# Kernel tuning notes

Hardware: AMD Instinct MI355X
Metric: run time of the kernel (lower is better)

## Reference

```python
import jax, jax.numpy as jnp
import numpy as np

N, E = 50000, 640000          # nodes, edges
F_IN, HID, CLS = 128, 128, 64  # feature dims


def setup_inputs() -> dict:
    key = jax.random.key(0)
    ks = jax.random.split(key, 12)
    x = jax.random.normal(ks[0], (N, F_IN), dtype=jnp.float32)
    edge_index = jax.random.randint(ks[1], (2, E), 0, N, dtype=jnp.int32)
    s_in = 1.0 / np.sqrt(F_IN)
    s_h = 1.0 / np.sqrt(HID)
    return {
        "x": x,
        "edge_index": edge_index,
        "W0": jax.random.normal(ks[2], (F_IN, HID), jnp.float32) * s_in,
        "b0": jnp.zeros((HID,), jnp.float32),
        "W1": jax.random.normal(ks[3], (HID, HID), jnp.float32) * s_h,
        "b1": jnp.zeros((HID,), jnp.float32),
        "W2": jax.random.normal(ks[4], (HID, HID), jnp.float32) * s_h,
        "b2": jnp.zeros((HID,), jnp.float32),
        "W_lin": jax.random.normal(ks[5], (HID, CLS), jnp.float32) * s_h,
        "b_lin": jnp.zeros((CLS,), jnp.float32),
    }


def reference(x, edge_index, W0, b0, W1, b1, W2, b2, W_lin, b_lin):
    # GCNConv (PyG defaults): out = D^-1/2 (A + I) D^-1/2 (x @ W) + b
    row, col = edge_index[0], edge_index[1]  # source -> target
    # degree with self-loop (graph is fixed across layers, compute norms once)
    deg = jnp.zeros((N,), x.dtype).at[col].add(1.0) + 1.0
    dinv = jax.lax.rsqrt(deg)                 # deg >= 1, safe
    enorm = (dinv[row] * dinv[col])[:, None]  # [E,1] edge norm
    snorm = (dinv * dinv)[:, None]            # [N,1] self-loop norm

    def conv(h, W, b):
        h = h @ W                                             # [N,HID]
        agg = jnp.zeros_like(h).at[col].add(h[row] * enorm)   # neighbor agg
        return agg + h * snorm + b                            # + self loop + bias

    h = jax.nn.relu(conv(x, W0, b0))
    h = jax.nn.relu(conv(h, W1, b1))
    h = jax.nn.relu(conv(h, W2, b2))
    return h @ W_lin + b_lin
```

## Files before the change

kernel.cpp:

```cpp
#include <hip/hip_runtime.h>
#include <hip/hip_fp16.h>

#define N_NODES 50000
#define HID 128
#define CLS 64

#define NBINS 196
#define NBLK 256
#define LBUF_CAP 4096
#define WTOT 57344
#define GEMM0_BLOCKS 782
#define AROW 136

typedef __attribute__((ext_vector_type(8))) _Float16 f16x8;
typedef __attribute__((ext_vector_type(4))) float f32x4;

__global__ __launch_bounds__(256) void hist_wsplit_kernel(
    const int* __restrict__ col, int* __restrict__ hist,
    const float* __restrict__ W0, const float* __restrict__ W1,
    const float* __restrict__ W2, const float* __restrict__ Wl,
    __half* __restrict__ o0h, __half* __restrict__ o0l,
    __half* __restrict__ o1h, __half* __restrict__ o1l,
    __half* __restrict__ o2h, __half* __restrict__ o2l,
    __half* __restrict__ o3h, __half* __restrict__ o3l,
    int E, int chunk) {
    int widx = blockIdx.x * 256 + threadIdx.x;
    if (widx < WTOT) {
        const float* W;
        __half *oh, *ol;
        int NCdim, local;
        if (widx < 16384)      { W = W0; oh = o0h; ol = o0l; NCdim = 128; local = widx; }
        else if (widx < 32768) { W = W1; oh = o1h; ol = o1l; NCdim = 128; local = widx - 16384; }
        else if (widx < 49152) { W = W2; oh = o2h; ol = o2l; NCdim = 128; local = widx - 32768; }
        else                   { W = Wl; oh = o3h; ol = o3l; NCdim = 64;  local = widx - 49152; }
        int nn = local >> 7;
        int k = local & 127;
        float v = W[(size_t)k * NCdim + nn];
        __half h = __float2half_rn(v);
        oh[local] = h;
        ol[local] = __float2half_rn(v - __half2float(h));
    }
    __shared__ int h[NBINS];
    for (int i = threadIdx.x; i < NBINS; i += 256) h[i] = 0;
    __syncthreads();
    int b = blockIdx.x;
    int beg = b * chunk;
    int end = min(E, beg + chunk);
    if (beg < end) {
        int vend = beg + ((end - beg) & ~3);
        for (int i = beg + threadIdx.x * 4; i < vend; i += 1024) {
            int4 c4 = *(const int4*)(col + i);
            atomicAdd(&h[c4.x >> 8], 1);
            atomicAdd(&h[c4.y >> 8], 1);
            atomicAdd(&h[c4.z >> 8], 1);
            atomicAdd(&h[c4.w >> 8], 1);
        }
        int i = vend + threadIdx.x;
        if (i < end) atomicAdd(&h[col[i] >> 8], 1);
    }
    __syncthreads();
    for (int i = threadIdx.x; i < NBINS; i += 256)
        hist[i * NBLK + b] = h[i];
}

__global__ __launch_bounds__(256) void binscan_kernel(
    const int* __restrict__ hist, int* __restrict__ cursorBase,
    int* __restrict__ binTotal) {
    __shared__ int ss[256];
    int bin = blockIdx.x, t = threadIdx.x;
    int v = hist[bin * NBLK + t];
    ss[t] = v;
    __syncthreads();
#pragma unroll
    for (int off = 1; off < 256; off <<= 1) {
        int u = (t >= off) ? ss[t - off] : 0;
        __syncthreads();
        ss[t] += u;
        __syncthreads();
    }
    cursorBase[bin * NBLK + t] = ss[t] - v;
    if (t == 255) binTotal[bin] = ss[255];
}

__global__ __launch_bounds__(256) void scatter_kernel(
    const int* __restrict__ row, const int* __restrict__ col,
    const int* __restrict__ binTotal, const int* __restrict__ cursorBase,
    int* __restrict__ binBase_g,
    unsigned short* __restrict__ sbuf_src, unsigned char* __restrict__ sbuf_c,
    int E, int chunk) {
    __shared__ int ss[256];
    __shared__ int cur[NBINS];
    int b = blockIdx.x, t = threadIdx.x;
    int v = (t < NBINS) ? binTotal[t] : 0;
    ss[t] = v;
    __syncthreads();
#pragma unroll
    for (int off = 1; off < 256; off <<= 1) {
        int u = (t >= off) ? ss[t - off] : 0;
        __syncthreads();
        ss[t] += u;
        __syncthreads();
    }
    int myBase = ss[t] - v;
    if (t < NBINS) cur[t] = myBase + cursorBase[t * NBLK + b];
    if (b == 0) {
        if (t < NBINS) binBase_g[t] = myBase;
        if (t == 0) binBase_g[NBINS] = E;
    }
    __syncthreads();
    int beg = b * chunk;
    int end = min(E, beg + chunk);
    if (beg >= end) return;
    int vend = beg + ((end - beg) & ~3);
    for (int i = beg + t * 4; i < vend; i += 1024) {
        int4 c4 = *(const int4*)(col + i);
        int4 r4 = *(const int4*)(row + i);
        int p;
        p = atomicAdd(&cur[c4.x >> 8], 1); sbuf_src[p] = (unsigned short)r4.x; sbuf_c[p] = (unsigned char)(c4.x & 255);
        p = atomicAdd(&cur[c4.y >> 8], 1); sbuf_src[p] = (unsigned short)r4.y; sbuf_c[p] = (unsigned char)(c4.y & 255);
        p = atomicAdd(&cur[c4.z >> 8], 1); sbuf_src[p] = (unsigned short)r4.z; sbuf_c[p] = (unsigned char)(c4.z & 255);
        p = atomicAdd(&cur[c4.w >> 8], 1); sbuf_src[p] = (unsigned short)r4.w; sbuf_c[p] = (unsigned char)(c4.w & 255);
    }
    int i = vend + t;
    if (i < end) {
        int c = col[i];
        int p = atomicAdd(&cur[c >> 8], 1);
        sbuf_src[p] = (unsigned short)row[i];
        sbuf_c[p] = (unsigned char)(c & 255);
    }
}

__device__ __forceinline__ void gemm0_body(
    const float* __restrict__ x, const __half* __restrict__ Bh,
    const __half* __restrict__ Bl, __half* __restrict__ C, int M, int rowTile) {
    constexpr int NT = 8;
    int lane = threadIdx.x & 63;
    int m0 = rowTile << 4;
    if (m0 >= M) return;
    int mr = lane & 15;
    int kq = (lane >> 4) << 3;

    const float*  af = x + (size_t)(m0 + mr) * 128 + kq;
    const __half* bh = Bh + (size_t)mr * 128 + kq;
    const __half* bl = Bl + (size_t)mr * 128 + kq;

    f32x4 acc[NT];
#pragma unroll
    for (int t = 0; t < NT; ++t) acc[t] = (f32x4){0.f, 0.f, 0.f, 0.f};
#pragma unroll
    for (int kc = 0; kc < 128; kc += 32) {
        float4 lo = *(const float4*)(af + kc);
        float4 hi = *(const float4*)(af + kc + 4);
        f16x8 a;
        a[0] = (_Float16)lo.x; a[1] = (_Float16)lo.y;
        a[2] = (_Float16)lo.z; a[3] = (_Float16)lo.w;
        a[4] = (_Float16)hi.x; a[5] = (_Float16)hi.y;
        a[6] = (_Float16)hi.z; a[7] = (_Float16)hi.w;
#pragma unroll
        for (int t = 0; t < NT; ++t) {
            f16x8 wh = *(const f16x8*)(bh + (size_t)t * 16 * 128 + kc);
            f16x8 wl = *(const f16x8*)(bl + (size_t)t * 16 * 128 + kc);
            acc[t] = __builtin_amdgcn_mfma_f32_16x16x32_f16(a, wh, acc[t], 0, 0, 0);
            acc[t] = __builtin_amdgcn_mfma_f32_16x16x32_f16(a, wl, acc[t], 0, 0, 0);
        }
    }
    int r0 = m0 + ((lane >> 4) << 2);
    int cc = lane & 15;
#pragma unroll
    for (int t = 0; t < NT; ++t)
#pragma unroll
        for (int r = 0; r < 4; ++r)
            C[(size_t)(r0 + r) * 128 + t * 16 + cc] =
                __float2half_rn(acc[t][r]);
}

__global__ __launch_bounds__(256) void csrplace_gemm0_kernel(
    const int* __restrict__ binBase,
    const unsigned short* __restrict__ sbuf_src, const unsigned char* __restrict__ sbuf_c,
    float* __restrict__ dinv, int* __restrict__ row_ptr,
    unsigned short* __restrict__ csr_src,
    const float* __restrict__ x, const __half* __restrict__ W0h,
    const __half* __restrict__ W0l, __half* __restrict__ h2, int n, int E) {
    __shared__ int lcnt[256];
    __shared__ int lcur[256];
    __shared__ int ss[256];
    __shared__ int lbuf[LBUF_CAP];
    int b = blockIdx.x;
    if (b >= NBINS) {
        gemm0_body(x, W0h, W0l, h2, n, (b - NBINS) * 4 + (threadIdx.x >> 6));
        return;
    }
    int t = threadIdx.x;
    lcnt[t] = 0;
    __syncthreads();
    int beg = binBase[b], end = binBase[b + 1];
    for (int j = beg + t; j < end; j += 256)
        atomicAdd(&lcnt[sbuf_c[j]], 1);
    __syncthreads();
    int deg = lcnt[t];
    int node = b * 256 + t;
    if (node < n) dinv[node] = rsqrtf((float)deg + 1.0f);
    ss[t] = deg;
    __syncthreads();
#pragma unroll
    for (int off = 1; off < 256; off <<= 1) {
        int u = (t >= off) ? ss[t - off] : 0;
        __syncthreads();
        ss[t] += u;
        __syncthreads();
    }
    int excl = ss[t] - deg;
    lcur[t] = excl;
    int total = ss[255];
    if (node < n) row_ptr[node] = beg + excl;
    if (b == 0 && t == 0) row_ptr[n] = E;
    __syncthreads();
    for (int j = beg + t; j < end; j += 256) {
        int c = sbuf_c[j];
        int pos = atomicAdd(&lcur[c], 1);
        lbuf[pos] = sbuf_src[j];
    }
    __syncthreads();
    for (int j = t; j < total; j += 256)
        csr_src[beg + j] = (unsigned short)lbuf[j];
}

template<int NC, bool HEAD>
__global__ __launch_bounds__(256) void agg_gemm_kernel(
    const __half* __restrict__ h2, const int* __restrict__ row_ptr,
    const unsigned short* __restrict__ csr_src, const float* __restrict__ dinv,
    const float* __restrict__ bias,
    const __half* __restrict__ Bh, const __half* __restrict__ Bl,
    const float* __restrict__ gbias, void* __restrict__ Cv, int n) {
    __shared__ __half Als[16][AROW];
    int wave = threadIdx.x >> 6;
    int lane = threadIdx.x & 63;
    int m0 = blockIdx.x << 4;

    int g = lane >> 4;
    int l16 = lane & 15;
    int baseLane = lane & 48;
    int lr = (wave << 2) + g;
    int wid = m0 + lr;
    const __half* hrow = h2 + (l16 << 3);

    if (wid < n) {
        int beg = row_ptr[wid];
        int end = row_ptr[wid + 1];
        float dv = dinv[wid];
        float acc[8];
#pragma unroll
        for (int i = 0; i < 8; ++i) acc[i] = 0.f;

        for (int base = beg; base < end; base += 16) {
            int cnt = end - base;
            if (cnt > 16) cnt = 16;
            int msrc = 0;
            float mw = 0.f;
            if (l16 < cnt) {
                msrc = csr_src[base + l16];
                mw = dinv[msrc] * dv;
            }
            int j = 0;
            for (; j + 4 <= cnt; j += 4) {
                int s0 = __shfl(msrc, baseLane + j);
                int s1 = __shfl(msrc, baseLane + j + 1);
                int s2 = __shfl(msrc, baseLane + j + 2);
                int s3 = __shfl(msrc, baseLane + j + 3);
                float w0 = __shfl(mw, baseLane + j);
                float w1 = __shfl(mw, baseLane + j + 1);
                float w2 = __shfl(mw, baseLane + j + 2);
                float w3 = __shfl(mw, baseLane + j + 3);
                f16x8 v0 = *(const f16x8*)(hrow + ((size_t)s0 << 7));
                f16x8 v1 = *(const f16x8*)(hrow + ((size_t)s1 << 7));
                f16x8 v2 = *(const f16x8*)(hrow + ((size_t)s2 << 7));
                f16x8 v3 = *(const f16x8*)(hrow + ((size_t)s3 << 7));
#pragma unroll
                for (int i = 0; i < 8; ++i) {
                    acc[i] = fmaf((float)v0[i], w0, acc[i]);
                    acc[i] = fmaf((float)v1[i], w1, acc[i]);
                    acc[i] = fmaf((float)v2[i], w2, acc[i]);
                    acc[i] = fmaf((float)v3[i], w3, acc[i]);
                }
            }
            for (; j + 2 <= cnt; j += 2) {
                int s0 = __shfl(msrc, baseLane + j);
                int s1 = __shfl(msrc, baseLane + j + 1);
                float w0 = __shfl(mw, baseLane + j);
                float w1 = __shfl(mw, baseLane + j + 1);
                f16x8 v0 = *(const f16x8*)(hrow + ((size_t)s0 << 7));
                f16x8 v1 = *(const f16x8*)(hrow + ((size_t)s1 << 7));
#pragma unroll
                for (int i = 0; i < 8; ++i) {
                    acc[i] = fmaf((float)v0[i], w0, acc[i]);
                    acc[i] = fmaf((float)v1[i], w1, acc[i]);
                }
            }
            if (j < cnt) {
                int s0 = __shfl(msrc, baseLane + j);
                float w0 = __shfl(mw, baseLane + j);
                f16x8 v0 = *(const f16x8*)(hrow + ((size_t)s0 << 7));
#pragma unroll
                for (int i = 0; i < 8; ++i)
                    acc[i] = fmaf((float)v0[i], w0, acc[i]);
            }
        }
        float sn = dv * dv;
        f16x8 sv = *(const f16x8*)(hrow + ((size_t)wid << 7));
        float4 ba = *(const float4*)(bias + (l16 << 3));
        float4 bb = *(const float4*)(bias + (l16 << 3) + 4);
        float o[8];
#pragma unroll
        for (int i = 0; i < 8; ++i) o[i] = fmaf((float)sv[i], sn, acc[i]);
        o[0] += ba.x; o[1] += ba.y; o[2] += ba.z; o[3] += ba.w;
        o[4] += bb.x; o[5] += bb.y; o[6] += bb.z; o[7] += bb.w;
        f16x8 pk;
#pragma unroll
        for (int i = 0; i < 8; ++i) pk[i] = (_Float16)fmaxf(o[i], 0.f);
        *(f16x8*)&Als[lr][l16 << 3] = pk;
    }
    __syncthreads();

    constexpr int NT = NC / 16;
    constexpr int TPW = NT / 4;
    int mr = lane & 15;
    int kq = (lane >> 4) << 3;
    const __half* bh = Bh + (size_t)mr * 128 + kq;
    const __half* bl = Bl + (size_t)mr * 128 + kq;

    f32x4 acc[TPW];
#pragma unroll
    for (int t = 0; t < TPW; ++t) acc[t] = (f32x4){0.f, 0.f, 0.f, 0.f};
#pragma unroll
    for (int kc = 0; kc < 128; kc += 32) {
        f16x8 a = *(const f16x8*)&Als[mr][kq + kc];
#pragma unroll
        for (int t = 0; t < TPW; ++t) {
            int tile = wave * TPW + t;
            f16x8 wh = *(const f16x8*)(bh + (size_t)tile * 16 * 128 + kc);
            f16x8 wl = *(const f16x8*)(bl + (size_t)tile * 16 * 128 + kc);
            acc[t] = __builtin_amdgcn_mfma_f32_16x16x32_f16(a, wh, acc[t], 0, 0, 0);
            acc[t] = __builtin_amdgcn_mfma_f32_16x16x32_f16(a, wl, acc[t], 0, 0, 0);
        }
    }
    int r0 = m0 + ((lane >> 4) << 2);
    int cc = lane & 15;
#pragma unroll
    for (int t = 0; t < TPW; ++t) {
        int tile = wave * TPW + t;
        float bsv = HEAD ? gbias[tile * 16 + cc] : 0.f;
#pragma unroll
        for (int r = 0; r < 4; ++r) {
            if (r0 + r >= n) break;
            size_t idx = (size_t)(r0 + r) * NC + tile * 16 + cc;
            float val = acc[t][r] + bsv;
            if (HEAD)
                ((float*)Cv)[idx] = val;
            else
                ((__half*)Cv)[idx] = __float2half_rn(val);
        }
    }
}

extern "C" void kernel_launch(void* const* d_in, const int* in_sizes, int n_in,
                              void* d_out, int out_size, void* d_ws, size_t ws_size,
                              hipStream_t stream) {
    const float* x  = (const float*)d_in[0];
    const int* ei   = (const int*)d_in[1];
    const float* W0 = (const float*)d_in[2];
    const float* b0 = (const float*)d_in[3];
    const float* W1 = (const float*)d_in[4];
    const float* b1 = (const float*)d_in[5];
    const float* W2 = (const float*)d_in[6];
    const float* b2 = (const float*)d_in[7];
    const float* Wl = (const float*)d_in[8];
    const float* bl = (const float*)d_in[9];
    float* out = (float*)d_out;

    const int N = N_NODES;
    const int E = in_sizes[1] / 2;
    const int* row = ei;
    const int* col = ei + E;
    const int chunk = (((E + NBLK - 1) / NBLK) + 3) & ~3;

    char* ws = (char*)d_ws;
    auto alloc = [&](size_t bytes) {
        char* p = ws;
        ws += (bytes + 255) & ~(size_t)255;
        return p;
    };
    int*   hist      = (int*)alloc((size_t)NBINS * NBLK * 4);
    int*   cursorBase= (int*)alloc((size_t)NBINS * NBLK * 4);
    int*   binTotal  = (int*)alloc((size_t)NBINS * 4);
    int*   binBase   = (int*)alloc((size_t)(NBINS + 1) * 4);
    unsigned short* sbuf_src = (unsigned short*)alloc((size_t)E * 2);
    unsigned char*  sbuf_c   = (unsigned char*)alloc((size_t)E);
    int*   row_ptr = (int*)alloc((size_t)(N + 1) * 4);
    float* dinv    = (float*)alloc((size_t)N * 4);
    unsigned short* csr_src = (unsigned short*)alloc((size_t)E * 2);
    __half* h2a    = (__half*)alloc((size_t)N * HID * 2);
    __half* h2b    = (__half*)alloc((size_t)N * HID * 2);
    __half* Wt_h[4];
    __half* Wt_l[4];
    for (int i = 0; i < 3; ++i) {
        Wt_h[i] = (__half*)alloc((size_t)HID * HID * 2);
        Wt_l[i] = (__half*)alloc((size_t)HID * HID * 2);
    }
    Wt_h[3] = (__half*)alloc((size_t)CLS * HID * 2);
    Wt_l[3] = (__half*)alloc((size_t)CLS * HID * 2);

    hist_wsplit_kernel<<<NBLK, 256, 0, stream>>>(col, hist, W0, W1, W2, Wl,
        Wt_h[0], Wt_l[0], Wt_h[1], Wt_l[1], Wt_h[2], Wt_l[2], Wt_h[3], Wt_l[3], E, chunk);
    binscan_kernel<<<NBINS, 256, 0, stream>>>(hist, cursorBase, binTotal);
    scatter_kernel<<<NBLK, 256, 0, stream>>>(row, col, binTotal, cursorBase,
        binBase, sbuf_src, sbuf_c, E, chunk);
    csrplace_gemm0_kernel<<<NBINS + GEMM0_BLOCKS, 256, 0, stream>>>(
        binBase, sbuf_src, sbuf_c, dinv, row_ptr, csr_src,
        x, Wt_h[0], Wt_l[0], h2a, N, E);

    const int fusedBlocks = (N + 15) / 16;

    agg_gemm_kernel<128, false><<<fusedBlocks, 256, 0, stream>>>(
        h2a, row_ptr, csr_src, dinv, b0, Wt_h[1], Wt_l[1], nullptr, h2b, N);
    agg_gemm_kernel<128, false><<<fusedBlocks, 256, 0, stream>>>(
        h2b, row_ptr, csr_src, dinv, b1, Wt_h[2], Wt_l[2], nullptr, h2a, N);
    agg_gemm_kernel<64, true><<<fusedBlocks, 256, 0, stream>>>(
        h2a, row_ptr, csr_src, dinv, b2, Wt_h[3], Wt_l[3], bl, out, N);
}
```

Baseline: 265.5 us.

## Replace binned two-level CSR build with global-atomic degree count and direct scatter

```diff
diff --git a/kernel.cpp b/kernel.cpp
--- a/kernel.cpp
+++ b/kernel.cpp
@@ -5,25 +5,24 @@
 #define HID 128
 #define CLS 64
 
-#define NBINS 196
-#define NBLK 256
-#define LBUF_CAP 4096
+#define NSCAN 196
 #define WTOT 57344
+#define SCAT_BLOCKS 256
 #define GEMM0_BLOCKS 782
 #define AROW 136
 
 typedef __attribute__((ext_vector_type(8))) _Float16 f16x8;
 typedef __attribute__((ext_vector_type(4))) float f32x4;
 
-__global__ __launch_bounds__(256) void hist_wsplit_kernel(
-    const int* __restrict__ col, int* __restrict__ hist,
+__global__ __launch_bounds__(256) void degcount_wsplit_kernel(
+    const int* __restrict__ col, int* __restrict__ deg,
     const float* __restrict__ W0, const float* __restrict__ W1,
     const float* __restrict__ W2, const float* __restrict__ Wl,
     __half* __restrict__ o0h, __half* __restrict__ o0l,
     __half* __restrict__ o1h, __half* __restrict__ o1l,
     __half* __restrict__ o2h, __half* __restrict__ o2l,
     __half* __restrict__ o3h, __half* __restrict__ o3l,
-    int E, int chunk) {
+    int E) {
     int widx = blockIdx.x * 256 + threadIdx.x;
     if (widx < WTOT) {
         const float* W;
@@ -40,35 +39,29 @@
         oh[local] = h;
         ol[local] = __float2half_rn(v - __half2float(h));
     }
-    __shared__ int h[NBINS];
-    for (int i = threadIdx.x; i < NBINS; i += 256) h[i] = 0;
-    __syncthreads();
-    int b = blockIdx.x;
-    int beg = b * chunk;
-    int end = min(E, beg + chunk);
-    if (beg < end) {
-        int vend = beg + ((end - beg) & ~3);
-        for (int i = beg + threadIdx.x * 4; i < vend; i += 1024) {
-            int4 c4 = *(const int4*)(col + i);
-            atomicAdd(&h[c4.x >> 8], 1);
-            atomicAdd(&h[c4.y >> 8], 1);
-            atomicAdd(&h[c4.z >> 8], 1);
-            atomicAdd(&h[c4.w >> 8], 1);
-        }
-        int i = vend + threadIdx.x;
-        if (i < end) atomicAdd(&h[col[i] >> 8], 1);
-    }
-    __syncthreads();
-    for (int i = threadIdx.x; i < NBINS; i += 256)
-        hist[i * NBLK + b] = h[i];
-}
-
-__global__ __launch_bounds__(256) void binscan_kernel(
-    const int* __restrict__ hist, int* __restrict__ cursorBase,
-    int* __restrict__ binTotal) {
+    int E4 = E & ~3;
+    int stride = 256 * 256 * 4;
+    for (int i = (blockIdx.x * 256 + threadIdx.x) * 4; i < E4; i += stride) {
+        int4 c4 = *(const int4*)(col + i);
+        atomicAdd(&deg[c4.x], 1);
+        atomicAdd(&deg[c4.y], 1);
+        atomicAdd(&deg[c4.z], 1);
+        atomicAdd(&deg[c4.w], 1);
+    }
+    if (blockIdx.x == 0) {
+        int r = E - E4;
+        if (threadIdx.x < r) atomicAdd(&deg[col[E4 + threadIdx.x]], 1);
+    }
+}
+
+__global__ __launch_bounds__(256) void scan_local_kernel(
+    const int* __restrict__ deg, int* __restrict__ rpl,
+    int* __restrict__ blockSum, float* __restrict__ dinv, int n) {
     __shared__ int ss[256];
-    int bin = blockIdx.x, t = threadIdx.x;
-    int v = hist[bin * NBLK + t];
+    int b = blockIdx.x, t = threadIdx.x;
+    int node = b * 256 + t;
+    int v = (node < n) ? deg[node] : 0;
+    if (node < n) dinv[node] = rsqrtf((float)v + 1.0f);
     ss[t] = v;
     __syncthreads();
 #pragma unroll
@@ -78,21 +71,19 @@
         ss[t] += u;
         __syncthreads();
     }
-    cursorBase[bin * NBLK + t] = ss[t] - v;
-    if (t == 255) binTotal[bin] = ss[255];
-}
-
-__global__ __launch_bounds__(256) void scatter_kernel(
-    const int* __restrict__ row, const int* __restrict__ col,
-    const int* __restrict__ binTotal, const int* __restrict__ cursorBase,
-    int* __restrict__ binBase_g,
-    unsigned short* __restrict__ sbuf_src, unsigned char* __restrict__ sbuf_c,
-    int E, int chunk) {
+    if (node < n) rpl[node] = ss[t] - v;
+    if (t == 255) blockSum[b] = ss[255];
+}
+
+__global__ __launch_bounds__(256) void scan_final_kernel(
+    const int* __restrict__ rpl, const int* __restrict__ blockSum,
+    int* __restrict__ row_ptr, int* __restrict__ cur, int n, int E) {
     __shared__ int ss[256];
-    __shared__ int cur[NBINS];
+    __shared__ int orig[256];
     int b = blockIdx.x, t = threadIdx.x;
-    int v = (t < NBINS) ? binTotal[t] : 0;
+    int v = (t < NSCAN) ? blockSum[t] : 0;
     ss[t] = v;
+    orig[t] = v;
     __syncthreads();
 #pragma unroll
     for (int off = 1; off < 256; off <<= 1) {
@@ -101,33 +92,14 @@
         ss[t] += u;
         __syncthreads();
     }
-    int myBase = ss[t] - v;
-    if (t < NBINS) cur[t] = myBase + cursorBase[t * NBLK + b];
-    if (b == 0) {
-        if (t < NBINS) binBase_g[t] = myBase;
-        if (t == 0) binBase_g[NBINS] = E;
-    }
-    __syncthreads();
-    int beg = b * chunk;
-    int end = min(E, beg + chunk);
-    if (beg >= end) return;
-    int vend = beg + ((end - beg) & ~3);
-    for (int i = beg + t * 4; i < vend; i += 1024) {
-        int4 c4 = *(const int4*)(col + i);
-        int4 r4 = *(const int4*)(row + i);
-        int p;
-        p = atomicAdd(&cur[c4.x >> 8], 1); sbuf_src[p] = (unsigned short)r4.x; sbuf_c[p] = (unsigned char)(c4.x & 255);
-        p = atomicAdd(&cur[c4.y >> 8], 1); sbuf_src[p] = (unsigned short)r4.y; sbuf_c[p] = (unsigned char)(c4.y & 255);
-        p = atomicAdd(&cur[c4.z >> 8], 1); sbuf_src[p] = (unsigned short)r4.z; sbuf_c[p] = (unsigned char)(c4.z & 255);
-        p = atomicAdd(&cur[c4.w >> 8], 1); sbuf_src[p] = (unsigned short)r4.w; sbuf_c[p] = (unsigned char)(c4.w & 255);
-    }
-    int i = vend + t;
-    if (i < end) {
-        int c = col[i];
-        int p = atomicAdd(&cur[c >> 8], 1);
-        sbuf_src[p] = (unsigned short)row[i];
-        sbuf_c[p] = (unsigned char)(c & 255);
-    }
+    int base = ss[b] - orig[b];
+    int node = b * 256 + t;
+    if (node < n) {
+        int r = rpl[node] + base;
+        row_ptr[node] = r;
+        cur[node] = r;
+    }
+    if (b == 0 && t == 0) row_ptr[n] = E;
 }
 
 __device__ __forceinline__ void gemm0_body(
@@ -174,55 +146,38 @@
                 __float2half_rn(acc[t][r]);
 }
 
-__global__ __launch_bounds__(256) void csrplace_gemm0_kernel(
-    const int* __restrict__ binBase,
-    const unsigned short* __restrict__ sbuf_src, const unsigned char* __restrict__ sbuf_c,
-    float* __restrict__ dinv, int* __restrict__ row_ptr,
-    unsigned short* __restrict__ csr_src,
+__global__ __launch_bounds__(256) void scatter_gemm0_kernel(
+    const int* __restrict__ row, const int* __restrict__ col,
+    int* __restrict__ cur, unsigned short* __restrict__ csr_src,
     const float* __restrict__ x, const __half* __restrict__ W0h,
     const __half* __restrict__ W0l, __half* __restrict__ h2, int n, int E) {
-    __shared__ int lcnt[256];
-    __shared__ int lcur[256];
-    __shared__ int ss[256];
-    __shared__ int lbuf[LBUF_CAP];
     int b = blockIdx.x;
-    if (b >= NBINS) {
-        gemm0_body(x, W0h, W0l, h2, n, (b - NBINS) * 4 + (threadIdx.x >> 6));
+    if (b >= SCAT_BLOCKS) {
+        gemm0_body(x, W0h, W0l, h2, n, (b - SCAT_BLOCKS) * 4 + (threadIdx.x >> 6));
         return;
     }
     int t = threadIdx.x;
-    lcnt[t] = 0;
-    __syncthreads();
-    int beg = binBase[b], end = binBase[b + 1];
-    for (int j = beg + t; j < end; j += 256)
-        atomicAdd(&lcnt[sbuf_c[j]], 1);
-    __syncthreads();
-    int deg = lcnt[t];
-    int node = b * 256 + t;
-    if (node < n) dinv[node] = rsqrtf((float)deg + 1.0f);
-    ss[t] = deg;
-    __syncthreads();
-#pragma unroll
-    for (int off = 1; off < 256; off <<= 1) {
-        int u = (t >= off) ? ss[t - off] : 0;
-        __syncthreads();
-        ss[t] += u;
-        __syncthreads();
-    }
-    int excl = ss[t] - deg;
-    lcur[t] = excl;
-    int total = ss[255];
-    if (node < n) row_ptr[node] = beg + excl;
-    if (b == 0 && t == 0) row_ptr[n] = E;
-    __syncthreads();
-    for (int j = beg + t; j < end; j += 256) {
-        int c = sbuf_c[j];
-        int pos = atomicAdd(&lcur[c], 1);
-        lbuf[pos] = sbuf_src[j];
-    }
-    __syncthreads();
-    for (int j = t; j < total; j += 256)
-        csr_src[beg + j] = (unsigned short)lbuf[j];
+    int E4 = E & ~3;
+    int stride = SCAT_BLOCKS * 256 * 4;
+    for (int i = (b * 256 + t) * 4; i < E4; i += stride) {
+        int4 c4 = *(const int4*)(col + i);
+        int4 r4 = *(const int4*)(row + i);
+        int p0 = atomicAdd(&cur[c4.x], 1);
+        int p1 = atomicAdd(&cur[c4.y], 1);
+        int p2 = atomicAdd(&cur[c4.z], 1);
+        int p3 = atomicAdd(&cur[c4.w], 1);
+        csr_src[p0] = (unsigned short)r4.x;
+        csr_src[p1] = (unsigned short)r4.y;
+        csr_src[p2] = (unsigned short)r4.z;
+        csr_src[p3] = (unsigned short)r4.w;
+    }
+    if (b == 0) {
+        int r = E - E4;
+        if (t < r) {
+            int p = atomicAdd(&cur[col[E4 + t]], 1);
+            csr_src[p] = (unsigned short)row[E4 + t];
+        }
+    }
 }
 
 template<int NC, bool HEAD>
@@ -381,7 +336,6 @@
     const int E = in_sizes[1] / 2;
     const int* row = ei;
     const int* col = ei + E;
-    const int chunk = (((E + NBLK - 1) / NBLK) + 3) & ~3;
 
     char* ws = (char*)d_ws;
     auto alloc = [&](size_t bytes) {
@@ -389,14 +343,12 @@
         ws += (bytes + 255) & ~(size_t)255;
         return p;
     };
-    int*   hist      = (int*)alloc((size_t)NBINS * NBLK * 4);
-    int*   cursorBase= (int*)alloc((size_t)NBINS * NBLK * 4);
-    int*   binTotal  = (int*)alloc((size_t)NBINS * 4);
-    int*   binBase   = (int*)alloc((size_t)(NBINS + 1) * 4);
-    unsigned short* sbuf_src = (unsigned short*)alloc((size_t)E * 2);
-    unsigned char*  sbuf_c   = (unsigned char*)alloc((size_t)E);
-    int*   row_ptr = (int*)alloc((size_t)(N + 1) * 4);
-    float* dinv    = (float*)alloc((size_t)N * 4);
+    int*   deg      = (int*)alloc((size_t)N * 4);
+    int*   rpl      = (int*)alloc((size_t)N * 4);
+    int*   blockSum = (int*)alloc((size_t)NSCAN * 4);
+    int*   row_ptr  = (int*)alloc((size_t)(N + 1) * 4);
+    int*   cur      = (int*)alloc((size_t)N * 4);
+    float* dinv     = (float*)alloc((size_t)N * 4);
     unsigned short* csr_src = (unsigned short*)alloc((size_t)E * 2);
     __half* h2a    = (__half*)alloc((size_t)N * HID * 2);
     __half* h2b    = (__half*)alloc((size_t)N * HID * 2);
@@ -409,14 +361,14 @@
     Wt_h[3] = (__half*)alloc((size_t)CLS * HID * 2);
     Wt_l[3] = (__half*)alloc((size_t)CLS * HID * 2);
 
-    hist_wsplit_kernel<<<NBLK, 256, 0, stream>>>(col, hist, W0, W1, W2, Wl,
-        Wt_h[0], Wt_l[0], Wt_h[1], Wt_l[1], Wt_h[2], Wt_l[2], Wt_h[3], Wt_l[3], E, chunk);
-    binscan_kernel<<<NBINS, 256, 0, stream>>>(hist, cursorBase, binTotal);
-    scatter_kernel<<<NBLK, 256, 0, stream>>>(row, col, binTotal, cursorBase,
-        binBase, sbuf_src, sbuf_c, E, chunk);
-    csrplace_gemm0_kernel<<<NBINS + GEMM0_BLOCKS, 256, 0, stream>>>(
-        binBase, sbuf_src, sbuf_c, dinv, row_ptr, csr_src,
-        x, Wt_h[0], Wt_l[0], h2a, N, E);
+    hipMemsetAsync(deg, 0, (size_t)N * 4, stream);
+
+    degcount_wsplit_kernel<<<256, 256, 0, stream>>>(col, deg, W0, W1, W2, Wl,
+        Wt_h[0], Wt_l[0], Wt_h[1], Wt_l[1], Wt_h[2], Wt_l[2], Wt_h[3], Wt_l[3], E);
+    scan_local_kernel<<<NSCAN, 256, 0, stream>>>(deg, rpl, blockSum, dinv, N);
+    scan_final_kernel<<<NSCAN, 256, 0, stream>>>(rpl, blockSum, row_ptr, cur, N, E);
+    scatter_gemm0_kernel<<<SCAT_BLOCKS + GEMM0_BLOCKS, 256, 0, stream>>>(
+        row, col, cur, csr_src, x, Wt_h[0], Wt_l[0], h2a, N, E);
 
     const int fusedBlocks = (N + 15) / 16;
 
```

Result: slower. 308.5 us (+16.2%).

## Move gemm0 blocks into histogram kernel and split weight conversion into own launch

Applied to the files above, without the earlier changes.

```diff
diff --git a/kernel.cpp b/kernel.cpp
--- a/kernel.cpp
+++ b/kernel.cpp
@@ -9,41 +9,93 @@
 #define NBLK 256
 #define LBUF_CAP 4096
 #define WTOT 57344
+#define WSPLIT_BLOCKS 224
 #define GEMM0_BLOCKS 782
 #define AROW 136
 
 typedef __attribute__((ext_vector_type(8))) _Float16 f16x8;
 typedef __attribute__((ext_vector_type(4))) float f32x4;
 
-__global__ __launch_bounds__(256) void hist_wsplit_kernel(
-    const int* __restrict__ col, int* __restrict__ hist,
+__global__ __launch_bounds__(256) void wsplit_kernel(
     const float* __restrict__ W0, const float* __restrict__ W1,
     const float* __restrict__ W2, const float* __restrict__ Wl,
     __half* __restrict__ o0h, __half* __restrict__ o0l,
     __half* __restrict__ o1h, __half* __restrict__ o1l,
     __half* __restrict__ o2h, __half* __restrict__ o2l,
-    __half* __restrict__ o3h, __half* __restrict__ o3l,
-    int E, int chunk) {
+    __half* __restrict__ o3h, __half* __restrict__ o3l) {
     int widx = blockIdx.x * 256 + threadIdx.x;
-    if (widx < WTOT) {
-        const float* W;
-        __half *oh, *ol;
-        int NCdim, local;
-        if (widx < 16384)      { W = W0; oh = o0h; ol = o0l; NCdim = 128; local = widx; }
-        else if (widx < 32768) { W = W1; oh = o1h; ol = o1l; NCdim = 128; local = widx - 16384; }
-        else if (widx < 49152) { W = W2; oh = o2h; ol = o2l; NCdim = 128; local = widx - 32768; }
-        else                   { W = Wl; oh = o3h; ol = o3l; NCdim = 64;  local = widx - 49152; }
-        int nn = local >> 7;
-        int k = local & 127;
-        float v = W[(size_t)k * NCdim + nn];
-        __half h = __float2half_rn(v);
-        oh[local] = h;
-        ol[local] = __float2half_rn(v - __half2float(h));
+    const float* W;
+    __half *oh, *ol;
+    int NCdim, local;
+    if (widx < 16384)      { W = W0; oh = o0h; ol = o0l; NCdim = 128; local = widx; }
+    else if (widx < 32768) { W = W1; oh = o1h; ol = o1l; NCdim = 128; local = widx - 16384; }
+    else if (widx < 49152) { W = W2; oh = o2h; ol = o2l; NCdim = 128; local = widx - 32768; }
+    else                   { W = Wl; oh = o3h; ol = o3l; NCdim = 64;  local = widx - 49152; }
+    int nn = local >> 7;
+    int k = local & 127;
+    float v = W[(size_t)k * NCdim + nn];
+    __half h = __float2half_rn(v);
+    oh[local] = h;
+    ol[local] = __float2half_rn(v - __half2float(h));
+}
+
+__device__ __forceinline__ void gemm0_body(
+    const float* __restrict__ x, const __half* __restrict__ Bh,
+    const __half* __restrict__ Bl, __half* __restrict__ C, int M, int rowTile) {
+    constexpr int NT = 8;
+    int lane = threadIdx.x & 63;
+    int m0 = rowTile << 4;
+    if (m0 >= M) return;
+    int mr = lane & 15;
+    int kq = (lane >> 4) << 3;
+
+    const float*  af = x + (size_t)(m0 + mr) * 128 + kq;
+    const __half* bh = Bh + (size_t)mr * 128 + kq;
+    const __half* bl = Bl + (size_t)mr * 128 + kq;
+
+    f32x4 acc[NT];
+#pragma unroll
+    for (int t = 0; t < NT; ++t) acc[t] = (f32x4){0.f, 0.f, 0.f, 0.f};
+#pragma unroll
+    for (int kc = 0; kc < 128; kc += 32) {
+        float4 lo = *(const float4*)(af + kc);
+        float4 hi = *(const float4*)(af + kc + 4);
+        f16x8 a;
+        a[0] = (_Float16)lo.x; a[1] = (_Float16)lo.y;
+        a[2] = (_Float16)lo.z; a[3] = (_Float16)lo.w;
+        a[4] = (_Float16)hi.x; a[5] = (_Float16)hi.y;
+        a[6] = (_Float16)hi.z; a[7] = (_Float16)hi.w;
+#pragma unroll
+        for (int t = 0; t < NT; ++t) {
+            f16x8 wh = *(const f16x8*)(bh + (size_t)t * 16 * 128 + kc);
+            f16x8 wl = *(const f16x8*)(bl + (size_t)t * 16 * 128 + kc);
+            acc[t] = __builtin_amdgcn_mfma_f32_16x16x32_f16(a, wh, acc[t], 0, 0, 0);
+            acc[t] = __builtin_amdgcn_mfma_f32_16x16x32_f16(a, wl, acc[t], 0, 0, 0);
+        }
+    }
+    int r0 = m0 + ((lane >> 4) << 2);
+    int cc = lane & 15;
+#pragma unroll
+    for (int t = 0; t < NT; ++t)
+#pragma unroll
+        for (int r = 0; r < 4; ++r)
+            C[(size_t)(r0 + r) * 128 + t * 16 + cc] =
+                __float2half_rn(acc[t][r]);
+}
+
+__global__ __launch_bounds__(256) void hist_gemm0_kernel(
+    const int* __restrict__ col, int* __restrict__ hist,
+    const float* __restrict__ x, const __half* __restrict__ W0h,
+    const __half* __restrict__ W0l, __half* __restrict__ h2,
+    int n, int E, int chunk) {
+    int b = blockIdx.x;
+    if (b >= NBLK) {
+        gemm0_body(x, W0h, W0l, h2, n, (b - NBLK) * 4 + (threadIdx.x >> 6));
+        return;
     }
     __shared__ int h[NBINS];
     for (int i = threadIdx.x; i < NBINS; i += 256) h[i] = 0;
     __syncthreads();
-    int b = blockIdx.x;
     int beg = b * chunk;
     int end = min(E, beg + chunk);
     if (beg < end) {
@@ -130,66 +182,16 @@
     }
 }
 
-__device__ __forceinline__ void gemm0_body(
-    const float* __restrict__ x, const __half* __restrict__ Bh,
-    const __half* __restrict__ Bl, __half* __restrict__ C, int M, int rowTile) {
-    constexpr int NT = 8;
-    int lane = threadIdx.x & 63;
-    int m0 = rowTile << 4;
-    if (m0 >= M) return;
-    int mr = lane & 15;
-    int kq = (lane >> 4) << 3;
-
-    const float*  af = x + (size_t)(m0 + mr) * 128 + kq;
-    const __half* bh = Bh + (size_t)mr * 128 + kq;
-    const __half* bl = Bl + (size_t)mr * 128 + kq;
-
-    f32x4 acc[NT];
-#pragma unroll
-    for (int t = 0; t < NT; ++t) acc[t] = (f32x4){0.f, 0.f, 0.f, 0.f};
-#pragma unroll
-    for (int kc = 0; kc < 128; kc += 32) {
-        float4 lo = *(const float4*)(af + kc);
-        float4 hi = *(const float4*)(af + kc + 4);
-        f16x8 a;
-        a[0] = (_Float16)lo.x; a[1] = (_Float16)lo.y;
-        a[2] = (_Float16)lo.z; a[3] = (_Float16)lo.w;
-        a[4] = (_Float16)hi.x; a[5] = (_Float16)hi.y;
-        a[6] = (_Float16)hi.z; a[7] = (_Float16)hi.w;
-#pragma unroll
-        for (int t = 0; t < NT; ++t) {
-            f16x8 wh = *(const f16x8*)(bh + (size_t)t * 16 * 128 + kc);
-            f16x8 wl = *(const f16x8*)(bl + (size_t)t * 16 * 128 + kc);
-            acc[t] = __builtin_amdgcn_mfma_f32_16x16x32_f16(a, wh, acc[t], 0, 0, 0);
-            acc[t] = __builtin_amdgcn_mfma_f32_16x16x32_f16(a, wl, acc[t], 0, 0, 0);
-        }
-    }
-    int r0 = m0 + ((lane >> 4) << 2);
-    int cc = lane & 15;
-#pragma unroll
-    for (int t = 0; t < NT; ++t)
-#pragma unroll
-        for (int r = 0; r < 4; ++r)
-            C[(size_t)(r0 + r) * 128 + t * 16 + cc] =
-                __float2half_rn(acc[t][r]);
-}
-
-__global__ __launch_bounds__(256) void csrplace_gemm0_kernel(
+__global__ __launch_bounds__(256) void csrplace_kernel(
     const int* __restrict__ binBase,
     const unsigned short* __restrict__ sbuf_src, const unsigned char* __restrict__ sbuf_c,
     float* __restrict__ dinv, int* __restrict__ row_ptr,
-    unsigned short* __restrict__ csr_src,
-    const float* __restrict__ x, const __half* __restrict__ W0h,
-    const __half* __restrict__ W0l, __half* __restrict__ h2, int n, int E) {
+    unsigned short* __restrict__ csr_src, int n, int E) {
     __shared__ int lcnt[256];
     __shared__ int lcur[256];
     __shared__ int ss[256];
     __shared__ int lbuf[LBUF_CAP];
     int b = blockIdx.x;
-    if (b >= NBINS) {
-        gemm0_body(x, W0h, W0l, h2, n, (b - NBINS) * 4 + (threadIdx.x >> 6));
-        return;
-    }
     int t = threadIdx.x;
     lcnt[t] = 0;
     __syncthreads();
@@ -409,14 +411,15 @@
     Wt_h[3] = (__half*)alloc((size_t)CLS * HID * 2);
     Wt_l[3] = (__half*)alloc((size_t)CLS * HID * 2);
 
-    hist_wsplit_kernel<<<NBLK, 256, 0, stream>>>(col, hist, W0, W1, W2, Wl,
-        Wt_h[0], Wt_l[0], Wt_h[1], Wt_l[1], Wt_h[2], Wt_l[2], Wt_h[3], Wt_l[3], E, chunk);
+    wsplit_kernel<<<WSPLIT_BLOCKS, 256, 0, stream>>>(W0, W1, W2, Wl,
+        Wt_h[0], Wt_l[0], Wt_h[1], Wt_l[1], Wt_h[2], Wt_l[2], Wt_h[3], Wt_l[3]);
+    hist_gemm0_kernel<<<NBLK + GEMM0_BLOCKS, 256, 0, stream>>>(
+        col, hist, x, Wt_h[0], Wt_l[0], h2a, N, E, chunk);
     binscan_kernel<<<NBINS, 256, 0, stream>>>(hist, cursorBase, binTotal);
     scatter_kernel<<<NBLK, 256, 0, stream>>>(row, col, binTotal, cursorBase,
         binBase, sbuf_src, sbuf_c, E, chunk);
-    csrplace_gemm0_kernel<<<NBINS + GEMM0_BLOCKS, 256, 0, stream>>>(
-        binBase, sbuf_src, sbuf_c, dinv, row_ptr, csr_src,
-        x, Wt_h[0], Wt_l[0], h2a, N, E);
+    csrplace_kernel<<<NBINS, 256, 0, stream>>>(
+        binBase, sbuf_src, sbuf_c, dinv, row_ptr, csr_src, N, E);
 
     const int fusedBlocks = (N + 15) / 16;
 
```

After: 280.2 us. +5.5%, slower.
